# Optimization experiments

Measured on AMD Instinct MI355X. Metric: run time of the kernel, lower is better.

The kernel has to match this reference:

```python
import jax, jax.numpy as jnp
import numpy as np

B, T, D_IN, D_OUT = 64, 1024, 512, 512


def setup_inputs() -> dict:
    key = jax.random.key(0)
    k_x, k_w, k_wr = jax.random.split(key, 3)
    x = jax.random.normal(k_x, (B, T, D_IN), dtype=jnp.float32)
    # glorot_uniform for W
    limit = np.sqrt(6.0 / (D_IN + D_OUT)).astype(np.float32)
    W = jax.random.uniform(k_w, (D_IN, D_OUT), dtype=jnp.float32, minval=-limit, maxval=limit)
    # orthogonal for W_recurrent
    a = jax.random.normal(k_wr, (D_OUT, D_OUT), dtype=jnp.float32)
    q, r = jnp.linalg.qr(a)
    W_recurrent = q * jnp.sign(jnp.diag(r))[None, :]
    b = jnp.zeros((D_OUT,), dtype=jnp.float32)
    return {"x": x, "W": W, "W_recurrent": W_recurrent, "b": b}


def reference(x, W, W_recurrent, b):
    # x: [B, T, D_in]; sequential tanh RNN; return last hidden state [B, D_out]
    x_t = jnp.transpose(x, (1, 0, 2))  # [T, B, D_in]
    h0 = jnp.zeros((x.shape[0], W.shape[1]), dtype=x.dtype)

    def step(h, xt):
        h_new = jnp.tanh(xt @ W + h @ W_recurrent + b)
        return h_new, None

    h_last, _ = jax.lax.scan(step, h0, x_t)
    return h_last
```

## Files before the change

### kernel.cpp

```cpp
#include <hip/hip_runtime.h>
#include <math.h>

#define BATCH   64
#define TSTEPS  1024
#define DIN     512
#define DH      512
#define MDIM    (BATCH * TSTEPS)

#define MB          16
#define HSTRIDE_W   260
#define H_WORDS     (16 * HSTRIDE_W)
#define SLICE_WORDS (16 * HSTRIDE_W)
#define WRL_WORDS   (8 * SLICE_WORDS)
#define K2_LDS_WORDS (WRL_WORDS + H_WORDS)
#define K2_LDS_BYTES (K2_LDS_WORDS * 4)

typedef _Float16 f16x8 __attribute__((ext_vector_type(8)));
typedef float    f32x4 __attribute__((ext_vector_type(4)));

__device__ inline unsigned short f2h_bits(float x) {
    _Float16 h = (_Float16)x;
    return __builtin_bit_cast(unsigned short, h);
}
__device__ inline float ftanh(float x) {
    float e = __builtin_amdgcn_exp2f(x * 2.88539008177792681472f);
    return 1.0f - 2.0f * __builtin_amdgcn_rcpf(e + 1.0f);
}

__global__ __launch_bounds__(256) void convert_x(const float* __restrict__ x,
                                                 _Float16* __restrict__ xh,
                                                 int nvec) {
    int i = blockIdx.x * blockDim.x + threadIdx.x;
    int stride = gridDim.x * blockDim.x;
    for (; i < nvec; i += stride) {
        const float4* p = (const float4*)x + 2 * (size_t)i;
        float4 a = p[0], b = p[1];
        f16x8 o = { (_Float16)a.x, (_Float16)a.y, (_Float16)a.z, (_Float16)a.w,
                    (_Float16)b.x, (_Float16)b.y, (_Float16)b.z, (_Float16)b.w };
        ((f16x8*)xh)[i] = o;
    }
}

__global__ __launch_bounds__(256) void transpose_w(const float* __restrict__ W,
                                                   _Float16* __restrict__ Wt) {
    __shared__ float tile[64][65];
    const int t  = threadIdx.x;
    const int c  = t & 63;
    const int r0 = t >> 6;
    const int bn = blockIdx.x & 7;
    const int bk = blockIdx.x >> 3;
    const int k0 = bk * 64, n0 = bn * 64;
    #pragma unroll
    for (int i = 0; i < 16; ++i)
        tile[r0 + 4 * i][c] = W[(size_t)(k0 + r0 + 4 * i) * DH + n0 + c];
    __syncthreads();
    #pragma unroll
    for (int i = 0; i < 16; ++i)
        Wt[(size_t)(n0 + r0 + 4 * i) * DIN + k0 + c] = (_Float16)tile[c][r0 + 4 * i];
}

__global__ __launch_bounds__(256) void gemm_xw_mfma(const _Float16* __restrict__ Xh,
                                                    const _Float16* __restrict__ Wt,
                                                    const float* __restrict__ bias,
                                                    float* __restrict__ XW) {
    __shared__ __align__(16) _Float16 Ah[128][32];
    __shared__ __align__(16) _Float16 Bh[128][32];

    const int tid  = threadIdx.x;
    const int wv   = tid >> 6;
    const int lane = tid & 63;
    const int bn   = blockIdx.x & 3;
    const int bm   = blockIdx.x >> 2;
    const int m0   = bm * 128;
    const int n0   = bn * 128;

    const int mbase = (wv >> 1) * 64;
    const int nbase = (wv & 1) * 64;
    const int fr    = lane & 15;
    const int fq    = lane >> 4;

    f32x4 acc[4][4];
    #pragma unroll
    for (int i = 0; i < 4; ++i)
        #pragma unroll
        for (int j = 0; j < 4; ++j)
            acc[i][j] = (f32x4){0.f, 0.f, 0.f, 0.f};

    for (int kc = 0; kc < DIN / 32; ++kc) {
        const int k0 = kc * 32;
#if __has_builtin(__builtin_amdgcn_global_load_lds)
        #pragma unroll
        for (int q = 0; q < 2; ++q) {
            const int rb = wv * 2 + q;
            const int gr = (rb * 16) + (lane >> 2);
            const int gc = (lane & 3) * 8;
            const _Float16* ga = Xh + (size_t)(m0 + gr) * DIN + k0 + gc;
            const _Float16* gb = Wt + (size_t)(n0 + gr) * DIN + k0 + gc;
            __builtin_amdgcn_global_load_lds(
                (const __attribute__((address_space(1))) void*)ga,
                (__attribute__((address_space(3))) void*)&Ah[rb * 16][0], 16, 0, 0);
            __builtin_amdgcn_global_load_lds(
                (const __attribute__((address_space(1))) void*)gb,
                (__attribute__((address_space(3))) void*)&Bh[rb * 16][0], 16, 0, 0);
        }
#else
        #pragma unroll
        for (int q = 0; q < 2; ++q) {
            const int h0 = (q * 256 + tid) * 8;
            const int row = h0 >> 5, col = h0 & 31;
            *((uint4*)Ah + (q * 256 + tid)) =
                *(const uint4*)(Xh + (size_t)(m0 + row) * DIN + k0 + col);
            *((uint4*)Bh + (q * 256 + tid)) =
                *(const uint4*)(Wt + (size_t)(n0 + row) * DIN + k0 + col);
        }
#endif
        __syncthreads();

        f16x8 af[4], bf[4];
        #pragma unroll
        for (int mt = 0; mt < 4; ++mt)
            af[mt] = *(const f16x8*)&Ah[mbase + mt * 16 + fr][fq * 8];
        #pragma unroll
        for (int nt = 0; nt < 4; ++nt)
            bf[nt] = *(const f16x8*)&Bh[nbase + nt * 16 + fr][fq * 8];
        #pragma unroll
        for (int mt = 0; mt < 4; ++mt)
            #pragma unroll
            for (int nt = 0; nt < 4; ++nt)
                acc[mt][nt] = __builtin_amdgcn_mfma_f32_16x16x32_f16(
                    af[mt], bf[nt], acc[mt][nt], 0, 0, 0);
        __syncthreads();
    }

    #pragma unroll
    for (int nt = 0; nt < 4; ++nt) {
        const int col = n0 + nbase + nt * 16 + fr;
        const float bvl = bias[col];
        #pragma unroll
        for (int mt = 0; mt < 4; ++mt) {
            #pragma unroll
            for (int r = 0; r < 4; ++r) {
                const int row = m0 + mbase + mt * 16 + fq * 4 + r;
                XW[(size_t)row * DH + col] = acc[mt][nt][r] + bvl;
            }
        }
    }
}

__global__ __launch_bounds__(256) void gemm_xw(const float* __restrict__ X,
                                               const float* __restrict__ W,
                                               const float* __restrict__ bias,
                                               float* __restrict__ XW) {
    __shared__ float As[16][68];
    __shared__ float Bs[16][68];
    const int tid = threadIdx.x;
    const int bx  = blockIdx.x & 7;
    const int by  = blockIdx.x >> 3;
    const int m0  = by * 64, n0 = bx * 64;
    const int ty = tid >> 4, tx = tid & 15;
    const int arow = tid >> 2, akq = (tid & 3) * 4;
    const int brow = tid >> 4, bcq = (tid & 15) * 4;
    float acc[4][4] = {{0.f}};
    for (int k0 = 0; k0 < DIN; k0 += 16) {
        float4 av = *(const float4*)&X[(size_t)(m0 + arow) * DIN + k0 + akq];
        float4 bv = *(const float4*)&W[(size_t)(k0 + brow) * DH + n0 + bcq];
        __syncthreads();
        As[akq + 0][arow] = av.x; As[akq + 1][arow] = av.y;
        As[akq + 2][arow] = av.z; As[akq + 3][arow] = av.w;
        *(float4*)&Bs[brow][bcq] = bv;
        __syncthreads();
        #pragma unroll
        for (int k = 0; k < 16; ++k) {
            float4 a = *(const float4*)&As[k][ty * 4];
            float4 b = *(const float4*)&Bs[k][tx * 4];
            float ar[4] = {a.x, a.y, a.z, a.w};
            float br[4] = {b.x, b.y, b.z, b.w};
            #pragma unroll
            for (int i = 0; i < 4; ++i)
                #pragma unroll
                for (int j = 0; j < 4; ++j)
                    acc[i][j] = fmaf(ar[i], br[j], acc[i][j]);
        }
    }
    float4 bv = *(const float4*)&bias[n0 + tx * 4];
    const float br[4] = {bv.x, bv.y, bv.z, bv.w};
    #pragma unroll
    for (int i = 0; i < 4; ++i) {
        float4 o;
        o.x = acc[i][0] + br[0]; o.y = acc[i][1] + br[1];
        o.z = acc[i][2] + br[2]; o.w = acc[i][3] + br[3];
        *(float4*)&XW[(size_t)(m0 + ty * 4 + i) * DH + n0 + tx * 4] = o;
    }
}

__global__ __launch_bounds__(512, 2) void rnn_scan4(const float* __restrict__ XW,
                                                    const float* __restrict__ Wr,
                                                    float* __restrict__ Hout) {
    extern __shared__ unsigned int lds[];
    unsigned int*   wrl = lds;
    unsigned int*   hb  = lds + WRL_WORDS;
    unsigned short* hsh = (unsigned short*)hb;

    const int tid  = threadIdx.x;
    const int wv   = tid >> 6;
    const int lane = tid & 63;
    const int fr   = lane & 15;
    const int fq   = lane >> 4;
    const int b0   = blockIdx.x * MB;

    for (int i = tid; i < H_WORDS; i += 512) hb[i] = 0u;

    f16x8 breg[3][16];
    #pragma unroll
    for (int s = 0; s < 3; ++s) {
        const int col = wv * 64 + s * 16 + fr;
        #pragma unroll
        for (int c = 0; c < 16; ++c) {
            const int k0 = c * 32 + fq * 8;
            f16x8 v;
            #pragma unroll
            for (int j = 0; j < 8; ++j)
                v[j] = (_Float16)Wr[(size_t)(k0 + j) * DH + col];
            breg[s][c] = v;
        }
    }
    {
        const int col = wv * 64 + 48 + fr;
        unsigned int* base = wrl + wv * SLICE_WORDS + fr * HSTRIDE_W + fq * 4;
        #pragma unroll
        for (int c = 0; c < 16; ++c) {
            const int k0 = c * 32 + fq * 8;
            f16x8 v;
            #pragma unroll
            for (int j = 0; j < 8; ++j)
                v[j] = (_Float16)Wr[(size_t)(k0 + j) * DH + col];
            *(uint4*)(base + c * 16) = __builtin_bit_cast(uint4, v);
        }
    }
    __syncthreads();

    const float* xwt = XW + (size_t)(b0 + fq * 4) * TSTEPS * DH + wv * 64 + fr;
    const unsigned int* abase = hb + fr * HSTRIDE_W + fq * 4;
    const unsigned int* bbase = wrl + wv * SLICE_WORDS + fr * HSTRIDE_W + fq * 4;

    #pragma unroll 1
    for (int t = 0; t < TSTEPS; ++t) {
        f32x4 cc[4];
        #pragma unroll
        for (int s = 0; s < 4; ++s) cc[s] = (f32x4){0.f, 0.f, 0.f, 0.f};

        #pragma unroll
        for (int c = 0; c < 16; ++c) {
            f16x8 af = __builtin_bit_cast(f16x8, *(const uint4*)(abase + c * 16));
            f16x8 bf = __builtin_bit_cast(f16x8, *(const uint4*)(bbase + c * 16));
            cc[0] = __builtin_amdgcn_mfma_f32_16x16x32_f16(af, breg[0][c], cc[0], 0, 0, 0);
            cc[1] = __builtin_amdgcn_mfma_f32_16x16x32_f16(af, breg[1][c], cc[1], 0, 0, 0);
            cc[2] = __builtin_amdgcn_mfma_f32_16x16x32_f16(af, breg[2][c], cc[2], 0, 0, 0);
            cc[3] = __builtin_amdgcn_mfma_f32_16x16x32_f16(af, bf,         cc[3], 0, 0, 0);
        }

        float xv[4][4];
        #pragma unroll
        for (int s = 0; s < 4; ++s)
            #pragma unroll
            for (int r = 0; r < 4; ++r)
                xv[s][r] = xwt[(size_t)r * TSTEPS * DH + (size_t)t * DH + s * 16];

        __syncthreads();

        #pragma unroll
        for (int s = 0; s < 4; ++s) {
            #pragma unroll
            for (int r = 0; r < 4; ++r) {
                float h = ftanh(cc[s][r] + xv[s][r]);
                hsh[(fq * 4 + r) * (HSTRIDE_W * 2) + wv * 64 + s * 16 + fr] = f2h_bits(h);
            }
        }
        __syncthreads();
    }

    {
        const int m  = tid >> 5;
        const int cb = (tid & 31) * 16;
        #pragma unroll
        for (int g = 0; g < 16; g += 8) {
            f16x8 v = __builtin_bit_cast(f16x8,
                *(const uint4*)(hsh + (size_t)m * (HSTRIDE_W * 2) + cb + g));
            float4 o0 = { (float)v[0], (float)v[1], (float)v[2], (float)v[3] };
            float4 o1 = { (float)v[4], (float)v[5], (float)v[6], (float)v[7] };
            *(float4*)&Hout[(size_t)(b0 + m) * DH + cb + g]     = o0;
            *(float4*)&Hout[(size_t)(b0 + m) * DH + cb + g + 4] = o1;
        }
    }
}

extern "C" void kernel_launch(void* const* d_in, const int* in_sizes, int n_in,
                              void* d_out, int out_size, void* d_ws, size_t ws_size,
                              hipStream_t stream) {
    const float* x  = (const float*)d_in[0];
    const float* W  = (const float*)d_in[1];
    const float* Wr = (const float*)d_in[2];
    const float* bv = (const float*)d_in[3];
    float* out = (float*)d_out;

    const size_t XW_BYTES = (size_t)MDIM * DH * sizeof(float);
    const size_t XH_BYTES = (size_t)MDIM * DIN * sizeof(_Float16);
    const size_t WT_BYTES = (size_t)DIN * DH * sizeof(_Float16);
    if (ws_size < XW_BYTES) return;

    float* xw = (float*)d_ws;

    hipFuncSetAttribute((const void*)rnn_scan4,
                        hipFuncAttributeMaxDynamicSharedMemorySize, K2_LDS_BYTES);

    if (ws_size >= XW_BYTES + XH_BYTES + WT_BYTES) {
        _Float16* xh = (_Float16*)((char*)d_ws + XW_BYTES);
        _Float16* wt = (_Float16*)((char*)d_ws + XW_BYTES + XH_BYTES);
        convert_x<<<dim3(2048), dim3(256), 0, stream>>>(x, xh, MDIM * DIN / 8);
        transpose_w<<<dim3(64), dim3(256), 0, stream>>>(W, wt);
        gemm_xw_mfma<<<dim3((MDIM / 128) * (DH / 128)), dim3(256), 0, stream>>>(
            xh, wt, bv, xw);
    } else {
        gemm_xw<<<dim3((MDIM / 64) * (DH / 64)), dim3(256), 0, stream>>>(x, W, bv, xw);
    }

    rnn_scan4<<<dim3(BATCH / MB), dim3(512), K2_LDS_BYTES, stream>>>(xw, Wr, out);
}
```

Baseline: 2.078 ms.

## Double-buffer RNN hidden state, store XW in fp16, stream Wr slice from global

The recurrent scan now ping-pongs between two LDS hidden-state buffers, so each step needs one barrier instead of two. The fourth Wr slice moves out of LDS and is read from a pre-transposed fp16 global copy with a one-step-ahead prefetch. The precomputed XW intermediate is written and read as fp16, halving its memory traffic, and the xw loads are issued before the MFMA loop to hide their latency. The fp32 fallback GEMM is removed, which adds fp16 rounding of XW and a larger workspace requirement.

```diff
diff --git a/kernel.cpp b/kernel.cpp
--- a/kernel.cpp
+++ b/kernel.cpp
@@ -7,13 +7,9 @@
 #define DH      512
 #define MDIM    (BATCH * TSTEPS)
 
-#define MB          16
-#define HSTRIDE_W   260
-#define H_WORDS     (16 * HSTRIDE_W)
-#define SLICE_WORDS (16 * HSTRIDE_W)
-#define WRL_WORDS   (8 * SLICE_WORDS)
-#define K2_LDS_WORDS (WRL_WORDS + H_WORDS)
-#define K2_LDS_BYTES (K2_LDS_WORDS * 4)
+#define MB     16
+#define HSTR   260
+#define HBUF_W (16 * HSTR)
 
 typedef _Float16 f16x8 __attribute__((ext_vector_type(8)));
 typedef float    f32x4 __attribute__((ext_vector_type(4)));
@@ -41,8 +37,8 @@
     }
 }
 
-__global__ __launch_bounds__(256) void transpose_w(const float* __restrict__ W,
-                                                   _Float16* __restrict__ Wt) {
+__global__ __launch_bounds__(256) void transpose_w(const float* __restrict__ In,
+                                                   _Float16* __restrict__ Out) {
     __shared__ float tile[64][65];
     const int t  = threadIdx.x;
     const int c  = t & 63;
@@ -52,17 +48,17 @@
     const int k0 = bk * 64, n0 = bn * 64;
     #pragma unroll
     for (int i = 0; i < 16; ++i)
-        tile[r0 + 4 * i][c] = W[(size_t)(k0 + r0 + 4 * i) * DH + n0 + c];
+        tile[r0 + 4 * i][c] = In[(size_t)(k0 + r0 + 4 * i) * DH + n0 + c];
     __syncthreads();
     #pragma unroll
     for (int i = 0; i < 16; ++i)
-        Wt[(size_t)(n0 + r0 + 4 * i) * DIN + k0 + c] = (_Float16)tile[c][r0 + 4 * i];
+        Out[(size_t)(n0 + r0 + 4 * i) * DIN + k0 + c] = (_Float16)tile[c][r0 + 4 * i];
 }
 
 __global__ __launch_bounds__(256) void gemm_xw_mfma(const _Float16* __restrict__ Xh,
                                                     const _Float16* __restrict__ Wt,
                                                     const float* __restrict__ bias,
-                                                    float* __restrict__ XW) {
+                                                    _Float16* __restrict__ XWh) {
     __shared__ __align__(16) _Float16 Ah[128][32];
     __shared__ __align__(16) _Float16 Bh[128][32];
 
@@ -141,65 +137,16 @@
             #pragma unroll
             for (int r = 0; r < 4; ++r) {
                 const int row = m0 + mbase + mt * 16 + fq * 4 + r;
-                XW[(size_t)row * DH + col] = acc[mt][nt][r] + bvl;
+                XWh[(size_t)row * DH + col] = (_Float16)(acc[mt][nt][r] + bvl);
             }
         }
     }
 }
 
-__global__ __launch_bounds__(256) void gemm_xw(const float* __restrict__ X,
-                                               const float* __restrict__ W,
-                                               const float* __restrict__ bias,
-                                               float* __restrict__ XW) {
-    __shared__ float As[16][68];
-    __shared__ float Bs[16][68];
-    const int tid = threadIdx.x;
-    const int bx  = blockIdx.x & 7;
-    const int by  = blockIdx.x >> 3;
-    const int m0  = by * 64, n0 = bx * 64;
-    const int ty = tid >> 4, tx = tid & 15;
-    const int arow = tid >> 2, akq = (tid & 3) * 4;
-    const int brow = tid >> 4, bcq = (tid & 15) * 4;
-    float acc[4][4] = {{0.f}};
-    for (int k0 = 0; k0 < DIN; k0 += 16) {
-        float4 av = *(const float4*)&X[(size_t)(m0 + arow) * DIN + k0 + akq];
-        float4 bv = *(const float4*)&W[(size_t)(k0 + brow) * DH + n0 + bcq];
-        __syncthreads();
-        As[akq + 0][arow] = av.x; As[akq + 1][arow] = av.y;
-        As[akq + 2][arow] = av.z; As[akq + 3][arow] = av.w;
-        *(float4*)&Bs[brow][bcq] = bv;
-        __syncthreads();
-        #pragma unroll
-        for (int k = 0; k < 16; ++k) {
-            float4 a = *(const float4*)&As[k][ty * 4];
-            float4 b = *(const float4*)&Bs[k][tx * 4];
-            float ar[4] = {a.x, a.y, a.z, a.w};
-            float br[4] = {b.x, b.y, b.z, b.w};
-            #pragma unroll
-            for (int i = 0; i < 4; ++i)
-                #pragma unroll
-                for (int j = 0; j < 4; ++j)
-                    acc[i][j] = fmaf(ar[i], br[j], acc[i][j]);
-        }
-    }
-    float4 bv = *(const float4*)&bias[n0 + tx * 4];
-    const float br[4] = {bv.x, bv.y, bv.z, bv.w};
-    #pragma unroll
-    for (int i = 0; i < 4; ++i) {
-        float4 o;
-        o.x = acc[i][0] + br[0]; o.y = acc[i][1] + br[1];
-        o.z = acc[i][2] + br[2]; o.w = acc[i][3] + br[3];
-        *(float4*)&XW[(size_t)(m0 + ty * 4 + i) * DH + n0 + tx * 4] = o;
-    }
-}
-
-__global__ __launch_bounds__(512, 2) void rnn_scan4(const float* __restrict__ XW,
-                                                    const float* __restrict__ Wr,
+__global__ __launch_bounds__(512, 2) void rnn_scan5(const _Float16* __restrict__ XWh,
+                                                    const _Float16* __restrict__ WrT,
                                                     float* __restrict__ Hout) {
-    extern __shared__ unsigned int lds[];
-    unsigned int*   wrl = lds;
-    unsigned int*   hb  = lds + WRL_WORDS;
-    unsigned short* hsh = (unsigned short*)hb;
+    __shared__ unsigned int hb[2 * HBUF_W];
 
     const int tid  = threadIdx.x;
     const int wv   = tid >> 6;
@@ -208,84 +155,74 @@
     const int fq   = lane >> 4;
     const int b0   = blockIdx.x * MB;
 
-    for (int i = tid; i < H_WORDS; i += 512) hb[i] = 0u;
-
     f16x8 breg[3][16];
     #pragma unroll
     for (int s = 0; s < 3; ++s) {
-        const int col = wv * 64 + s * 16 + fr;
-        #pragma unroll
-        for (int c = 0; c < 16; ++c) {
-            const int k0 = c * 32 + fq * 8;
-            f16x8 v;
-            #pragma unroll
-            for (int j = 0; j < 8; ++j)
-                v[j] = (_Float16)Wr[(size_t)(k0 + j) * DH + col];
-            breg[s][c] = v;
-        }
-    }
-    {
-        const int col = wv * 64 + 48 + fr;
-        unsigned int* base = wrl + wv * SLICE_WORDS + fr * HSTRIDE_W + fq * 4;
-        #pragma unroll
-        for (int c = 0; c < 16; ++c) {
-            const int k0 = c * 32 + fq * 8;
-            f16x8 v;
-            #pragma unroll
-            for (int j = 0; j < 8; ++j)
-                v[j] = (_Float16)Wr[(size_t)(k0 + j) * DH + col];
-            *(uint4*)(base + c * 16) = __builtin_bit_cast(uint4, v);
-        }
-    }
+        const _Float16* pb = WrT + (size_t)(wv * 64 + s * 16 + fr) * DIN + fq * 8;
+        #pragma unroll
+        for (int c = 0; c < 16; ++c)
+            breg[s][c] = *(const f16x8*)(pb + c * 32);
+    }
+    const _Float16* p3 = WrT + (size_t)(wv * 64 + 48 + fr) * DIN + fq * 8;
+
+    for (int i = tid; i < 2 * HBUF_W; i += 512) hb[i] = 0u;
     __syncthreads();
 
-    const float* xwt = XW + (size_t)(b0 + fq * 4) * TSTEPS * DH + wv * 64 + fr;
-    const unsigned int* abase = hb + fr * HSTRIDE_W + fq * 4;
-    const unsigned int* bbase = wrl + wv * SLICE_WORDS + fr * HSTRIDE_W + fq * 4;
-
+    const _Float16* xwp = XWh + (size_t)(b0 + fq * 4) * TSTEPS * DH + wv * 64 + fr;
+    const unsigned int* ab0 = hb + fr * HSTR + fq * 4;
+    const unsigned int* ab1 = ab0 + HBUF_W;
+
+    int cur = 0;
     #pragma unroll 1
     for (int t = 0; t < TSTEPS; ++t) {
+        const unsigned int* ab = cur ? ab1 : ab0;
+
+        float xv[4][4];
+        #pragma unroll
+        for (int s = 0; s < 4; ++s)
+            #pragma unroll
+            for (int r = 0; r < 4; ++r)
+                xv[s][r] = (float)xwp[(size_t)r * TSTEPS * DH + (size_t)t * DH + s * 16];
+
         f32x4 cc[4];
         #pragma unroll
         for (int s = 0; s < 4; ++s) cc[s] = (f32x4){0.f, 0.f, 0.f, 0.f};
 
+        f16x8 bcur = *(const f16x8*)(p3 + 0 * 32);
+        f16x8 bnxt = *(const f16x8*)(p3 + 1 * 32);
+
         #pragma unroll
         for (int c = 0; c < 16; ++c) {
-            f16x8 af = __builtin_bit_cast(f16x8, *(const uint4*)(abase + c * 16));
-            f16x8 bf = __builtin_bit_cast(f16x8, *(const uint4*)(bbase + c * 16));
+            f16x8 af = __builtin_bit_cast(f16x8, *(const uint4*)(ab + c * 16));
             cc[0] = __builtin_amdgcn_mfma_f32_16x16x32_f16(af, breg[0][c], cc[0], 0, 0, 0);
             cc[1] = __builtin_amdgcn_mfma_f32_16x16x32_f16(af, breg[1][c], cc[1], 0, 0, 0);
             cc[2] = __builtin_amdgcn_mfma_f32_16x16x32_f16(af, breg[2][c], cc[2], 0, 0, 0);
-            cc[3] = __builtin_amdgcn_mfma_f32_16x16x32_f16(af, bf,         cc[3], 0, 0, 0);
-        }
-
-        float xv[4][4];
-        #pragma unroll
-        for (int s = 0; s < 4; ++s)
-            #pragma unroll
-            for (int r = 0; r < 4; ++r)
-                xv[s][r] = xwt[(size_t)r * TSTEPS * DH + (size_t)t * DH + s * 16];
-
-        __syncthreads();
-
+            cc[3] = __builtin_amdgcn_mfma_f32_16x16x32_f16(af, bcur,       cc[3], 0, 0, 0);
+            bcur = bnxt;
+            if (c + 2 < 16) bnxt = *(const f16x8*)(p3 + (c + 2) * 32);
+        }
+
+        unsigned short* hn = (unsigned short*)(hb + (cur ^ 1) * HBUF_W);
         #pragma unroll
         for (int s = 0; s < 4; ++s) {
             #pragma unroll
             for (int r = 0; r < 4; ++r) {
                 float h = ftanh(cc[s][r] + xv[s][r]);
-                hsh[(fq * 4 + r) * (HSTRIDE_W * 2) + wv * 64 + s * 16 + fr] = f2h_bits(h);
+                hn[(fq * 4 + r) * (HSTR * 2) + wv * 64 + s * 16 + fr] = f2h_bits(h);
             }
         }
         __syncthreads();
+        cur ^= 1;
     }
 
     {
+        const unsigned short* hf = (const unsigned short*)(hb + cur * HBUF_W);
         const int m  = tid >> 5;
         const int cb = (tid & 31) * 16;
         #pragma unroll
         for (int g = 0; g < 16; g += 8) {
             f16x8 v = __builtin_bit_cast(f16x8,
-                *(const uint4*)(hsh + (size_t)m * (HSTRIDE_W * 2) + cb + g));
+                *(const uint4*)(hf + (size_t)m * (HSTR * 2) + cb + g));
             float4 o0 = { (float)v[0], (float)v[1], (float)v[2], (float)v[3] };
             float4 o1 = { (float)v[4], (float)v[5], (float)v[6], (float)v[7] };
             *(float4*)&Hout[(size_t)(b0 + m) * DH + cb + g]     = o0;
@@ -303,26 +240,20 @@
     const float* bv = (const float*)d_in[3];
     float* out = (float*)d_out;
 
-    const size_t XW_BYTES = (size_t)MDIM * DH * sizeof(float);
-    const size_t XH_BYTES = (size_t)MDIM * DIN * sizeof(_Float16);
-    const size_t WT_BYTES = (size_t)DIN * DH * sizeof(_Float16);
-    if (ws_size < XW_BYTES) return;
-
-    float* xw = (float*)d_ws;
-
-    hipFuncSetAttribute((const void*)rnn_scan4,
-                        hipFuncAttributeMaxDynamicSharedMemorySize, K2_LDS_BYTES);
-
-    if (ws_size >= XW_BYTES + XH_BYTES + WT_BYTES) {
-        _Float16* xh = (_Float16*)((char*)d_ws + XW_BYTES);
-        _Float16* wt = (_Float16*)((char*)d_ws + XW_BYTES + XH_BYTES);
-        convert_x<<<dim3(2048), dim3(256), 0, stream>>>(x, xh, MDIM * DIN / 8);
-        transpose_w<<<dim3(64), dim3(256), 0, stream>>>(W, wt);
-        gemm_xw_mfma<<<dim3((MDIM / 128) * (DH / 128)), dim3(256), 0, stream>>>(
-            xh, wt, bv, xw);
-    } else {
-        gemm_xw<<<dim3((MDIM / 64) * (DH / 64)), dim3(256), 0, stream>>>(x, W, bv, xw);
-    }
-
-    rnn_scan4<<<dim3(BATCH / MB), dim3(512), K2_LDS_BYTES, stream>>>(xw, Wr, out);
-}
+    const size_t XWH_BYTES = (size_t)MDIM * DH * sizeof(_Float16);
+    const size_t XH_BYTES  = (size_t)MDIM * DIN * sizeof(_Float16);
+    const size_t WT_BYTES  = (size_t)DIN * DH * sizeof(_Float16);
+    if (ws_size < XWH_BYTES + XH_BYTES + 2 * WT_BYTES) return;
+
+    _Float16* xwh = (_Float16*)d_ws;
+    _Float16* xh  = (_Float16*)((char*)d_ws + XWH_BYTES);
+    _Float16* wt  = (_Float16*)((char*)d_ws + XWH_BYTES + XH_BYTES);
+    _Float16* wrt = (_Float16*)((char*)d_ws + XWH_BYTES + XH_BYTES + WT_BYTES);
+
+    convert_x<<<dim3(2048), dim3(256), 0, stream>>>(x, xh, MDIM * DIN / 8);
+    transpose_w<<<dim3(64), dim3(256), 0, stream>>>(W, wt);
+    transpose_w<<<dim3(64), dim3(256), 0, stream>>>(Wr, wrt);
+    gemm_xw_mfma<<<dim3((MDIM / 128) * (DH / 128)), dim3(256), 0, stream>>>(
+        xh, wt, bv, xwh);
+    rnn_scan5<<<dim3(BATCH / MB), dim3(512), 0, stream>>>(xwh, wrt, out);
+}
```

Result: slower. 4.516 ms (+117.3%).
